# Optimization experiments

Measured on AMD Instinct MI355X. Metric: run time of the kernel, lower is better.

The kernel has to match this reference:

```python
import jax, jax.numpy as jnp
import numpy as np

N_NODES = 100000
N_EDGES = 640000
IN_CH = 128
HID = 128


def setup_inputs() -> dict:
    key = jax.random.key(0)
    k1, k2, k3, k4, k5 = jax.random.split(key, 5)
    z = jax.random.normal(k1, (N_NODES, IN_CH), dtype=jnp.float32)
    edge_index = jax.random.randint(k2, (2, N_EDGES), 0, N_NODES, dtype=jnp.int64)
    # Linear layers: stored as [in, out] for x @ W + b
    s1 = 1.0 / np.sqrt(2 * IN_CH)
    W1 = jax.random.uniform(k3, (2 * IN_CH, HID), minval=-s1, maxval=s1, dtype=jnp.float32)
    b1 = jnp.zeros((HID,), dtype=jnp.float32)
    s2 = 1.0 / np.sqrt(HID)
    W2 = jax.random.uniform(k4, (HID, 1), minval=-s2, maxval=s2, dtype=jnp.float32)
    b2 = jnp.zeros((1,), dtype=jnp.float32)
    return {"z": z, "edge_index": edge_index, "W1": W1, "b1": b1, "W2": W2, "b2": b2}


def reference(z, edge_index, W1, b1, W2, b2):
    # gather source/destination node embeddings and concat -> [E, 2*C]
    h = jnp.concatenate([z[edge_index[0]], z[edge_index[1]]], axis=-1)
    h = jax.nn.relu(h @ W1 + b1)  # [E, HID]; Dropout(0.2) is identity in eval
    out = h @ W2 + b2             # [E, 1]
    return out.squeeze(-1)        # [E]
```

## Files before the change

kernel.cpp:

```cpp
#include <hip/hip_runtime.h>
#include <hip/hip_bf16.h>

typedef short bf16x8 __attribute__((ext_vector_type(8)));
typedef float f32x4  __attribute__((ext_vector_type(4)));
typedef unsigned short u16;

static __device__ __forceinline__ u16 f2bf(float f) {
    unsigned u = __float_as_uint(f);
    u += 0x7FFFu + ((u >> 16) & 1u);
    return (u16)(u >> 16);
}
static __device__ __forceinline__ float bf2f(u16 b) {
    return __uint_as_float(((unsigned)b) << 16);
}
static __device__ __forceinline__ unsigned pack2(float lo, float hi) {
    return (unsigned)f2bf(lo) | ((unsigned)f2bf(hi) << 16);
}

__global__ void prep_w(const float* __restrict__ W1, u16* __restrict__ Wl) {
    int idx = blockIdx.x * 256 + threadIdx.x;
    if (idx >= 256 * 128) return;
    int r = idx >> 7;
    int q = idx & 127;
    int k = (r < 128) ? r : (r - 128);
    int c = (r < 128) ? q : (q + 128);
    Wl[c * 128 + k] = f2bf(W1[idx]);
}

#define BM 64
__global__ __launch_bounds__(256, 2) void node_gemm(
    const float* __restrict__ z,
    const u16*   __restrict__ Wl,
    const float* __restrict__ b1,
    u16*         __restrict__ PQ,
    int M, int ntiles)
{
    __shared__ char As[2][BM * 256];
    const int tid  = threadIdx.x;
    const int lane = tid & 63;
    const int wave = tid >> 6;
    const int g    = lane >> 4;
    const int ln   = lane & 15;
    const int c0   = wave * 64;

    int t = blockIdx.x;
    if (t >= ntiles) return;

    float4 bias[4];
    #pragma unroll
    for (int ci = 0; ci < 4; ++ci) {
        int col = c0 + ci * 16 + g * 4;
        bias[ci] = (col < 128) ? *(const float4*)(b1 + col)
                               : make_float4(0.f, 0.f, 0.f, 0.f);
    }

    float4 r[8];

    {
        int m0 = t * BM;
        #pragma unroll
        for (int i = 0; i < 8; ++i) {
            int ci = tid + i * 256, row = ci >> 5, c4 = ci & 31;
            r[i] = make_float4(0.f, 0.f, 0.f, 0.f);
            if (m0 + row < M)
                r[i] = *(const float4*)(z + (size_t)(m0 + row) * 128 + c4 * 4);
        }
        #pragma unroll
        for (int i = 0; i < 8; ++i) {
            int ci = tid + i * 256, row = ci >> 5, c4 = ci & 31;
            ushort4 b;
            b.x = f2bf(r[i].x); b.y = f2bf(r[i].y);
            b.z = f2bf(r[i].z); b.w = f2bf(r[i].w);
            *(ushort4*)(As[0] + row * 256 + ((c4 * 8) ^ ((row & 7) << 4))) = b;
        }
    }
    __syncthreads();

    int cur = 0;
    while (true) {
        int next = t + gridDim.x;
        bool have = (next < ntiles);

        if (have) {
            int m0 = next * BM;
            #pragma unroll
            for (int i = 0; i < 8; ++i) {
                int ci = tid + i * 256, row = ci >> 5, c4 = ci & 31;
                r[i] = make_float4(0.f, 0.f, 0.f, 0.f);
                if (m0 + row < M)
                    r[i] = *(const float4*)(z + (size_t)(m0 + row) * 128 + c4 * 4);
            }
        }

        f32x4 acc[4][4];
        #pragma unroll
        for (int mf = 0; mf < 4; ++mf)
            #pragma unroll
            for (int ci = 0; ci < 4; ++ci)
                acc[mf][ci] = (f32x4){0.f, 0.f, 0.f, 0.f};

        #pragma unroll
        for (int ks = 0; ks < 4; ++ks) {
            bf16x8 a[4];
            #pragma unroll
            for (int ci = 0; ci < 4; ++ci)
                a[ci] = *(const bf16x8*)(Wl + (c0 + ci * 16 + ln) * 128 + ks * 32 + g * 8);
            #pragma unroll
            for (int mf = 0; mf < 4; ++mf) {
                int row  = mf * 16 + ln;
                int byte = row * 256 + ((ks * 64 + g * 16) ^ ((row & 7) << 4));
                bf16x8 b = *(const bf16x8*)(As[cur] + byte);
                #pragma unroll
                for (int ci = 0; ci < 4; ++ci)
                    acc[mf][ci] = __builtin_amdgcn_mfma_f32_16x16x32_bf16(
                        a[ci], b, acc[mf][ci], 0, 0, 0);
            }
        }

        if (have) {
            #pragma unroll
            for (int i = 0; i < 8; ++i) {
                int ci = tid + i * 256, row = ci >> 5, c4 = ci & 31;
                ushort4 b;
                b.x = f2bf(r[i].x); b.y = f2bf(r[i].y);
                b.z = f2bf(r[i].z); b.w = f2bf(r[i].w);
                *(ushort4*)(As[cur ^ 1] + row * 256 + ((c4 * 8) ^ ((row & 7) << 4))) = b;
            }
        }

        {
            int m0 = t * BM;
            #pragma unroll
            for (int mf = 0; mf < 4; ++mf) {
                int node = m0 + mf * 16 + ln;
                if (node < M) {
                    #pragma unroll
                    for (int ci = 0; ci < 4; ++ci) {
                        uint2 w;
                        w.x = pack2(acc[mf][ci][0] + bias[ci].x,
                                    acc[mf][ci][1] + bias[ci].y);
                        w.y = pack2(acc[mf][ci][2] + bias[ci].z,
                                    acc[mf][ci][3] + bias[ci].w);
                        *(uint2*)(PQ + (size_t)node * 256 + c0 + ci * 16 + g * 4) = w;
                    }
                }
            }
        }

        if (!have) break;
        __syncthreads();
        cur ^= 1;
        t = next;
    }
}

__global__ __launch_bounds__(256) void edge_mlp(
    const int* __restrict__ ei,
    const u16* __restrict__ PQ,
    const float* __restrict__ W2,
    const float* __restrict__ b2,
    float* __restrict__ out,
    int E)
{
    int gid = blockIdx.x * 256 + threadIdx.x;
    int e0  = (gid >> 4) * 4;
    int sub = gid & 15;
    if (e0 >= E) return;

    float4 w2a = *(const float4*)(W2 + sub * 8);
    float4 w2b = *(const float4*)(W2 + sub * 8 + 4);
    float ww[8] = {w2a.x, w2a.y, w2a.z, w2a.w, w2b.x, w2b.y, w2b.z, w2b.w};
    float bias = b2[0];

    if (e0 + 3 < E) {
        int4 s = *(const int4*)(ei + e0);
        int4 d = *(const int4*)(ei + E + e0);
        uint4 p0 = *(const uint4*)(PQ + (size_t)s.x * 256 + sub * 8);
        uint4 p1 = *(const uint4*)(PQ + (size_t)s.y * 256 + sub * 8);
        uint4 p2 = *(const uint4*)(PQ + (size_t)s.z * 256 + sub * 8);
        uint4 p3 = *(const uint4*)(PQ + (size_t)s.w * 256 + sub * 8);
        uint4 q0 = *(const uint4*)(PQ + (size_t)d.x * 256 + 128 + sub * 8);
        uint4 q1 = *(const uint4*)(PQ + (size_t)d.y * 256 + 128 + sub * 8);
        uint4 q2 = *(const uint4*)(PQ + (size_t)d.z * 256 + 128 + sub * 8);
        uint4 q3 = *(const uint4*)(PQ + (size_t)d.w * 256 + 128 + sub * 8);

        float a0 = 0.f, a1 = 0.f, a2 = 0.f, a3 = 0.f;
        const u16* pu0 = (const u16*)&p0; const u16* qu0 = (const u16*)&q0;
        const u16* pu1 = (const u16*)&p1; const u16* qu1 = (const u16*)&q1;
        const u16* pu2 = (const u16*)&p2; const u16* qu2 = (const u16*)&q2;
        const u16* pu3 = (const u16*)&p3; const u16* qu3 = (const u16*)&q3;
        #pragma unroll
        for (int j = 0; j < 8; ++j) {
            a0 = fmaf(fmaxf(bf2f(pu0[j]) + bf2f(qu0[j]), 0.f), ww[j], a0);
            a1 = fmaf(fmaxf(bf2f(pu1[j]) + bf2f(qu1[j]), 0.f), ww[j], a1);
            a2 = fmaf(fmaxf(bf2f(pu2[j]) + bf2f(qu2[j]), 0.f), ww[j], a2);
            a3 = fmaf(fmaxf(bf2f(pu3[j]) + bf2f(qu3[j]), 0.f), ww[j], a3);
        }
        #pragma unroll
        for (int m = 1; m < 16; m <<= 1) {
            a0 += __shfl_xor(a0, m);
            a1 += __shfl_xor(a1, m);
            a2 += __shfl_xor(a2, m);
            a3 += __shfl_xor(a3, m);
        }
        if (sub == 0) {
            float4 o = make_float4(a0 + bias, a1 + bias, a2 + bias, a3 + bias);
            *(float4*)(out + e0) = o;
        }
    } else {
        for (int k = 0; k < 4; ++k) {
            int e = e0 + k;
            if (e >= E) break;
            int sn = ei[e], dn = ei[E + e];
            uint4 p = *(const uint4*)(PQ + (size_t)sn * 256 + sub * 8);
            uint4 q = *(const uint4*)(PQ + (size_t)dn * 256 + 128 + sub * 8);
            const u16* pu = (const u16*)&p; const u16* qu = (const u16*)&q;
            float a = 0.f;
            #pragma unroll
            for (int j = 0; j < 8; ++j)
                a = fmaf(fmaxf(bf2f(pu[j]) + bf2f(qu[j]), 0.f), ww[j], a);
            #pragma unroll
            for (int m = 1; m < 16; m <<= 1) a += __shfl_xor(a, m);
            if (sub == 0) out[e] = a + bias;
        }
    }
}

extern "C" void kernel_launch(void* const* d_in, const int* in_sizes, int n_in,
                              void* d_out, int out_size, void* d_ws, size_t ws_size,
                              hipStream_t stream) {
    const float* z  = (const float*)d_in[0];
    const int*   ei = (const int*)d_in[1];
    const float* W1 = (const float*)d_in[2];
    const float* b1 = (const float*)d_in[3];
    const float* W2 = (const float*)d_in[4];
    const float* b2 = (const float*)d_in[5];
    float* out = (float*)d_out;

    const int M = in_sizes[0] / 128;
    const int E = in_sizes[1] / 2;

    u16* Wl = (u16*)d_ws;
    u16* PQ = (u16*)((char*)d_ws + 65536);

    hipLaunchKernelGGL(prep_w, dim3(128), dim3(256), 0, stream, W1, Wl);

    int ntiles = (M + BM - 1) / BM;
    int gb = ntiles < 512 ? ntiles : 512;
    hipLaunchKernelGGL(node_gemm, dim3(gb), dim3(256), 0, stream,
                       z, Wl, b1, PQ, M, ntiles);

    int eb = ((E + 3) / 4 * 16 + 255) / 256;
    hipLaunchKernelGGL(edge_mlp, dim3(eb), dim3(256), 0, stream,
                       ei, PQ, W2, b2, out, E);
}
```

Measured before the change: 80.97 us.

## Stage node GEMM output through LDS for coalesced stores and hoist weight fragments

The node GEMM output tile is written into a swizzled LDS buffer and then stored to global memory as full 16-byte row chunks, replacing the scattered 8-byte stores. The W1 bf16 fragments for all k-steps are loaded once into registers before the tile loop instead of being reloaded each tile. The A tile moves from double to single buffering, which adds a barrier between compute and the next tile's LDS write. The hoisted fragments raise register pressure, and the extra barrier and LDS traffic may hurt overlap.

Measured after the change: 74.13 us. -8.4%, faster.

```diff
diff --git a/kernel.cpp b/kernel.cpp
--- a/kernel.cpp
+++ b/kernel.cpp
@@ -35,7 +35,8 @@
     u16*         __restrict__ PQ,
     int M, int ntiles)
 {
-    __shared__ char As[2][BM * 256];
+    __shared__ char As[BM * 256];
+    __shared__ char Cb[BM * 512];
     const int tid  = threadIdx.x;
     const int lane = tid & 63;
     const int wave = tid >> 6;
@@ -46,6 +47,13 @@
     int t = blockIdx.x;
     if (t >= ntiles) return;
 
+    bf16x8 af[4][4];
+    #pragma unroll
+    for (int ks = 0; ks < 4; ++ks)
+        #pragma unroll
+        for (int ci = 0; ci < 4; ++ci)
+            af[ks][ci] = *(const bf16x8*)(Wl + (c0 + ci * 16 + ln) * 128 + ks * 32 + g * 8);
+
     float4 bias[4];
     #pragma unroll
     for (int ci = 0; ci < 4; ++ci) {
@@ -71,12 +79,11 @@
             ushort4 b;
             b.x = f2bf(r[i].x); b.y = f2bf(r[i].y);
             b.z = f2bf(r[i].z); b.w = f2bf(r[i].w);
-            *(ushort4*)(As[0] + row * 256 + ((c4 * 8) ^ ((row & 7) << 4))) = b;
+            *(ushort4*)(As + row * 256 + ((c4 * 8) ^ ((row & 7) << 4))) = b;
         }
     }
     __syncthreads();
 
-    int cur = 0;
     while (true) {
         int next = t + gridDim.x;
         bool have = (next < ntiles);
@@ -98,22 +105,47 @@
             #pragma unroll
             for (int ci = 0; ci < 4; ++ci)
                 acc[mf][ci] = (f32x4){0.f, 0.f, 0.f, 0.f};
-
         #pragma unroll
         for (int ks = 0; ks < 4; ++ks) {
-            bf16x8 a[4];
-            #pragma unroll
-            for (int ci = 0; ci < 4; ++ci)
-                a[ci] = *(const bf16x8*)(Wl + (c0 + ci * 16 + ln) * 128 + ks * 32 + g * 8);
             #pragma unroll
             for (int mf = 0; mf < 4; ++mf) {
                 int row  = mf * 16 + ln;
                 int byte = row * 256 + ((ks * 64 + g * 16) ^ ((row & 7) << 4));
-                bf16x8 b = *(const bf16x8*)(As[cur] + byte);
+                bf16x8 b = *(const bf16x8*)(As + byte);
                 #pragma unroll
                 for (int ci = 0; ci < 4; ++ci)
                     acc[mf][ci] = __builtin_amdgcn_mfma_f32_16x16x32_bf16(
-                        a[ci], b, acc[mf][ci], 0, 0, 0);
+                        af[ks][ci], b, acc[mf][ci], 0, 0, 0);
+            }
+        }
+
+        #pragma unroll
+        for (int mf = 0; mf < 4; ++mf) {
+            int node = mf * 16 + ln;
+            #pragma unroll
+            for (int ci = 0; ci < 4; ++ci) {
+                int col = c0 + ci * 16 + g * 4;
+                uint2 w;
+                w.x = pack2(acc[mf][ci][0] + bias[ci].x,
+                            acc[mf][ci][1] + bias[ci].y);
+                w.y = pack2(acc[mf][ci][2] + bias[ci].z,
+                            acc[mf][ci][3] + bias[ci].w);
+                *(uint2*)(Cb + node * 512 + ((col * 2) ^ ((node & 7) << 4))) = w;
+            }
+        }
+        __syncthreads();
+
+        {
+            int m0 = t * BM;
+            int chunk = tid & 31;
+            int nb    = tid >> 5;
+            #pragma unroll
+            for (int it = 0; it < 8; ++it) {
+                int node = it * 8 + nb;
+                uint4 v = *(const uint4*)(Cb + node * 512 +
+                                          ((chunk * 16) ^ ((node & 7) << 4)));
+                if (m0 + node < M)
+                    *(uint4*)(PQ + (size_t)(m0 + node) * 256 + chunk * 8) = v;
             }
         }
 
@@ -124,32 +156,12 @@
                 ushort4 b;
                 b.x = f2bf(r[i].x); b.y = f2bf(r[i].y);
                 b.z = f2bf(r[i].z); b.w = f2bf(r[i].w);
-                *(ushort4*)(As[cur ^ 1] + row * 256 + ((c4 * 8) ^ ((row & 7) << 4))) = b;
-            }
-        }
-
-        {
-            int m0 = t * BM;
-            #pragma unroll
-            for (int mf = 0; mf < 4; ++mf) {
-                int node = m0 + mf * 16 + ln;
-                if (node < M) {
-                    #pragma unroll
-                    for (int ci = 0; ci < 4; ++ci) {
-                        uint2 w;
-                        w.x = pack2(acc[mf][ci][0] + bias[ci].x,
-                                    acc[mf][ci][1] + bias[ci].y);
-                        w.y = pack2(acc[mf][ci][2] + bias[ci].z,
-                                    acc[mf][ci][3] + bias[ci].w);
-                        *(uint2*)(PQ + (size_t)node * 256 + c0 + ci * 16 + g * 4) = w;
-                    }
-                }
-            }
-        }
-
-        if (!have) break;
+                *(ushort4*)(As + row * 256 + ((c4 * 8) ^ ((row & 7) << 4))) = b;
+            }
+        } else {
+            break;
+        }
         __syncthreads();
-        cur ^= 1;
         t = next;
     }
 }
```
